# Optimization experiments

Measured on AMD Instinct MI355X. Metric: run time of the kernel, lower is better.

Reference implementation:

```python
import jax, jax.numpy as jnp
import numpy as np

N = 100000   # nodes
E = 1600000  # edges
IN = 32      # in_channels
H = 64       # hidden_channels
L = 16       # latent_dim
G = 64       # graphs in batch


def setup_inputs() -> dict:
    key = jax.random.key(0)
    ks = jax.random.split(key, 20)
    def w(k, shape, fan):
        return jax.random.normal(k, shape, jnp.float32) * (1.0 / np.sqrt(fan))
    inp = {}
    inp["x"] = jax.random.normal(ks[0], (N, IN), jnp.float32)
    inp["edge_index"] = jax.random.randint(ks[1], (2, E), 0, N)
    inp["batch"] = jnp.sort(jax.random.randint(ks[2], (N,), 0, G))
    # encoder GCN convs: in->h, h->h, h->h
    inp["W_enc0"] = w(ks[3], (IN, H), IN); inp["b_enc0"] = jnp.zeros((H,), jnp.float32)
    inp["W_enc1"] = w(ks[4], (H, H), H);   inp["b_enc1"] = jnp.zeros((H,), jnp.float32)
    inp["W_enc2"] = w(ks[5], (H, H), H);   inp["b_enc2"] = jnp.zeros((H,), jnp.float32)
    # latent projection and decoder projection
    inp["W_proj"] = w(ks[6], (H, L), H);   inp["b_proj"] = jnp.zeros((L,), jnp.float32)
    inp["W_dec_proj"] = w(ks[7], (L, H), L); inp["b_dec_proj"] = jnp.zeros((H,), jnp.float32)
    # decoder GCN convs: h->h, h->in
    inp["W_dec0"] = w(ks[8], (H, H), H);   inp["b_dec0"] = jnp.zeros((H,), jnp.float32)
    inp["W_dec1"] = w(ks[9], (H, IN), H);  inp["b_dec1"] = jnp.zeros((IN,), jnp.float32)
    return inp


def gcn_conv(x, W, b, src, dst, dinv):
    xw = x @ W                                   # [N, out]
    coef = (dinv[src] * dinv[dst])[:, None]      # [E, 1]
    out = jax.ops.segment_sum(xw[src] * coef, dst, num_segments=N)
    out = out + xw * (dinv * dinv)[:, None]      # self-loop contribution
    return out + b


def reference(x, edge_index, batch,
              W_enc0, b_enc0, W_enc1, b_enc1, W_enc2, b_enc2,
              W_proj, b_proj, W_dec_proj, b_dec_proj,
              W_dec0, b_dec0, W_dec1, b_dec1):
    src, dst = edge_index[0], edge_index[1]
    # degree with self-loops (computed on target nodes, PyG default)
    deg = jax.ops.segment_sum(jnp.ones((E,), jnp.float32), dst, num_segments=N) + 1.0
    dinv = jax.lax.rsqrt(deg)
    # encoder (eval mode: dropout is identity)
    h = jax.nn.relu(gcn_conv(x, W_enc0, b_enc0, src, dst, dinv))
    h = jax.nn.relu(gcn_conv(h, W_enc1, b_enc1, src, dst, dinv))
    h = jax.nn.relu(gcn_conv(h, W_enc2, b_enc2, src, dst, dinv))
    # global mean pool over graph ids
    sums = jax.ops.segment_sum(h, batch, num_segments=G)
    cnt = jax.ops.segment_sum(jnp.ones((N,), jnp.float32), batch, num_segments=G)
    g = sums / jnp.maximum(cnt, 1.0)[:, None]    # [G, H]
    z = g @ W_proj + b_proj                      # [G, L]
    # decoder: broadcast z back to nodes, project, two GCN convs
    d = jax.nn.relu(z[batch] @ W_dec_proj + b_dec_proj)
    d = jax.nn.relu(gcn_conv(d, W_dec0, b_dec0, src, dst, dinv))
    x_recon = gcn_conv(d, W_dec1, b_dec1, src, dst, dinv)
    return (x_recon, z)
```

## Files before the change

kernel.cpp:

```cpp
#include <hip/hip_runtime.h>
#include <hip/hip_bf16.h>

typedef unsigned long long u64;

static constexpr int IN_CH  = 32;
static constexpr int HID    = 64;
static constexpr int LAT    = 16;
static constexpr int NGRAPH = 64;
static constexpr int NBUCKET = 1024;
static constexpr int KB_CSR  = 24;


__device__ inline void add4(float4& a, const float4& b) {
    a.x += b.x; a.y += b.y; a.z += b.z; a.w += b.w;
}
__device__ inline float4 shfl_xor_f4(float4 v, int mask) {
    float4 r;
    r.x = __shfl_xor(v.x, mask);
    r.y = __shfl_xor(v.y, mask);
    r.z = __shfl_xor(v.z, mask);
    r.w = __shfl_xor(v.w, mask);
    return r;
}


__global__ __launch_bounds__(256) void bhist_kernel(const int* __restrict__ ei,
                                                    int* __restrict__ bh, int E) {
    __shared__ int lh[256];
    lh[threadIdx.x] = 0;
    __syncthreads();
    int base = blockIdx.x * 2048;
    #pragma unroll
    for (int j = 0; j < 8; j++) {
        int idx = base + j * 256 + threadIdx.x;
        if (idx < E) atomicAdd(&lh[ei[E + idx] >> 9], 1);
    }
    __syncthreads();
    if (lh[threadIdx.x]) atomicAdd(&bh[threadIdx.x], lh[threadIdx.x]);
}

__global__ __launch_bounds__(256) void bscan_kernel(const int* __restrict__ bh,
                                                    int* __restrict__ bbase, int E) {
    __shared__ int s[256];
    int t = threadIdx.x;
    int v = bh[t];
    s[t] = v;
    for (int off = 1; off < 256; off <<= 1) {
        __syncthreads();
        int x = (t >= off) ? s[t - off] : 0;
        __syncthreads();
        s[t] += x;
    }
    __syncthreads();
    bbase[t] = s[t] - v;
    if (t == 255) bbase[256] = E;
}


template <int MODE>
__global__ __launch_bounds__(256) void bin_kernel(
        const int* __restrict__ ei, const u64* __restrict__ sin,
        const int* __restrict__ rank,
        const int* __restrict__ bbase, int* __restrict__ gcur,
        u64* __restrict__ sout, int E) {
    __shared__ int lhist[256], lscan[256], lcur[256], gbase[256];
    __shared__ u64 sbuf[2048];
    int tid = threadIdx.x;
    lhist[tid] = 0;
    __syncthreads();
    int base = blockIdx.x * 2048;
    int cnt = min(2048, E - base);
    int myb[8]; u64 myp[8];
    #pragma unroll
    for (int j = 0; j < 8; j++) {
        int idx = base + j * 256 + tid;
        myb[j] = -1;
        if (idx < E) {
            int key, val;
            if constexpr (MODE == 0) { key = ei[E + idx]; val = ei[idx]; }
            else {
                u64 p = sin[idx];
                key = rank[(int)(p >> 32)];
                val = rank[(int)(p & 0xffffffffu)];
            }
            int b = key >> 9;
            myb[j] = b;
            myp[j] = ((u64)(unsigned)key << 32) | (unsigned)val;
            atomicAdd(&lhist[b], 1);
        }
    }
    __syncthreads();
    int v = lhist[tid];
    lscan[tid] = v;
    for (int off = 1; off < 256; off <<= 1) {
        __syncthreads();
        int x = (tid >= off) ? lscan[tid - off] : 0;
        __syncthreads();
        lscan[tid] += x;
    }
    __syncthreads();
    int excl = lscan[tid] - v;
    __syncthreads();
    lscan[tid] = excl;
    lcur[tid] = excl;
    __syncthreads();
    #pragma unroll
    for (int j = 0; j < 8; j++) {
        if (myb[j] >= 0) {
            int pos = atomicAdd(&lcur[myb[j]], 1);
            sbuf[pos] = myp[j];
        }
    }
    gbase[tid] = v ? atomicAdd(&gcur[tid], v) : 0;
    __syncthreads();
    for (int i = tid; i < cnt; i += 256) {
        u64 p = sbuf[i];
        int b = (int)(p >> 41);
        sout[bbase[b] + gbase[b] + (i - lscan[b])] = p;
    }
}


__global__ __launch_bounds__(256) void degb_kernel(
        const u64* __restrict__ staged, const int* __restrict__ bbase,
        int* __restrict__ cnt, int* __restrict__ hist, int N) {
    __shared__ int ldeg[512];
    __shared__ int lhist[NBUCKET];
    int b = blockIdx.x;
    ldeg[threadIdx.x] = 0;
    ldeg[threadIdx.x + 256] = 0;
    for (int i = threadIdx.x; i < NBUCKET; i += 256) lhist[i] = 0;
    __syncthreads();
    int s0 = bbase[b], s1 = bbase[b + 1];
    for (int i = s0 + threadIdx.x; i < s1; i += 256)
        atomicAdd(&ldeg[(int)(staged[i] >> 32) - (b << 9)], 1);
    __syncthreads();
    #pragma unroll
    for (int j = 0; j < 2; j++) {
        int t = threadIdx.x + j * 256;
        int n = (b << 9) + t;
        if (n < N) {
            int d = ldeg[t];
            cnt[n] = d;
            atomicAdd(&lhist[min(d, NBUCKET - 1)], 1);
        }
    }
    __syncthreads();
    for (int i = threadIdx.x; i < NBUCKET; i += 256)
        if (lhist[i]) atomicAdd(&hist[i], lhist[i]);
}

__global__ __launch_bounds__(1024) void hscan_kernel(int* hist) {
    __shared__ int s[NBUCKET];
    int t = threadIdx.x;
    int v = hist[t];
    s[t] = v;
    for (int off = 1; off < NBUCKET; off <<= 1) {
        __syncthreads();
        int x = (t >= off) ? s[t - off] : 0;
        __syncthreads();
        s[t] += x;
    }
    hist[t] = s[t] - v;
}

__global__ __launch_bounds__(256) void scatter_kernel(
        const int* __restrict__ cnt, const int* __restrict__ batch,
        const int* __restrict__ hoff, int* __restrict__ hcur,
        int* __restrict__ perm, int* __restrict__ rank, int* __restrict__ cnt2,
        float* __restrict__ dinvR, float2* __restrict__ pgR, int N) {
    __shared__ int lh[NBUCKET];
    __shared__ int gb[NBUCKET];
    for (int i = threadIdx.x; i < NBUCKET; i += 256) lh[i] = 0;
    __syncthreads();
    int n = blockIdx.x * 256 + threadIdx.x;
    int b = -1, lpos = 0, d = 0;
    if (n < N) {
        d = cnt[n];
        b = min(d, NBUCKET - 1);
        lpos = atomicAdd(&lh[b], 1);
    }
    __syncthreads();
    for (int i = threadIdx.x; i < NBUCKET; i += 256)
        gb[i] = lh[i] ? atomicAdd(&hcur[i], lh[i]) : 0;
    __syncthreads();
    if (n < N) {
        int r = hoff[b] + gb[b] + lpos;
        perm[r] = n;
        rank[n] = r;
        cnt2[r] = d;
        float dv = rsqrtf((float)d + 1.0f);
        dinvR[r] = dv;
        pgR[r] = make_float2(dv, __int_as_float(batch[n]));
    }
}


__global__ void scan1_kernel(const int* __restrict__ cnt, int* __restrict__ rowptr,
                             int* __restrict__ bsum, int N) {
    __shared__ int s[256];
    int i = blockIdx.x * 256 + threadIdx.x;
    int v = (i < N) ? cnt[i] : 0;
    s[threadIdx.x] = v;
    for (int off = 1; off < 256; off <<= 1) {
        __syncthreads();
        int t = (threadIdx.x >= off) ? s[threadIdx.x - off] : 0;
        __syncthreads();
        s[threadIdx.x] += t;
    }
    if (i < N) rowptr[i] = s[threadIdx.x] - v;
    if (threadIdx.x == 255) bsum[blockIdx.x] = s[255];
}

__global__ __launch_bounds__(512) void scan2_kernel(int* bsum, int nb) {
    __shared__ int s[512];
    int t = threadIdx.x;
    int v = (t < nb) ? bsum[t] : 0;
    s[t] = v;
    for (int off = 1; off < 512; off <<= 1) {
        __syncthreads();
        int x = (t >= off) ? s[t - off] : 0;
        __syncthreads();
        s[t] += x;
    }
    if (t < nb) bsum[t] = s[t] - v;
}

__global__ void scan3_kernel(int* __restrict__ rowptr, const int* __restrict__ bsum,
                             int* __restrict__ bbaseR, int N, int E) {
    int i = blockIdx.x * 256 + threadIdx.x;
    if (i < N) {
        int v = rowptr[i] + bsum[blockIdx.x];
        rowptr[i] = v;
        if ((i & 511) == 0) bbaseR[i >> 9] = v;
    }
    if (i == 0) {
        for (int t = (N + 511) >> 9; t <= 256; ++t) bbaseR[t] = E;
    }
}


__global__ __launch_bounds__(256) void csr_kernel(
        const u64* __restrict__ staged, const int* __restrict__ bbase,
        const int* __restrict__ rowptr2, int* __restrict__ cur,
        int* __restrict__ col) {
    int bucket = blockIdx.x & 255;
    int k = blockIdx.x >> 8;
    int s0 = bbase[bucket], s1 = bbase[bucket + 1];
    for (int i = s0 + k * 256 + threadIdx.x; i < s1; i += 256 * KB_CSR) {
        u64 p = staged[i];
        int r = (int)(p >> 32);
        int pos = rowptr2[r] + atomicAdd(&cur[r], 1);
        col[pos] = (int)(p & 0xffffffffu);
    }
}


__global__ void slice_x_kernel(const float* __restrict__ x, const int* __restrict__ perm,
                               const float* __restrict__ dinvR,
                               float* __restrict__ xs, int N) {
    int idx = blockIdx.x * 256 + threadIdx.x;
    if (idx >= N * 2) return;
    int r = idx >> 1, h = idx & 1;
    int sl = blockIdx.y;
    int n = perm[r];
    float4 v = ((const float4*)x)[(size_t)n * 8 + sl * 2 + h];
    float dn = dinvR[r];
    v.x *= dn; v.y *= dn; v.z *= dn; v.w *= dn;
    ((float4*)(xs + (size_t)sl * N * 8))[idx] = v;
}


template <int C, bool ADD_BIAS, bool OUT_ROWMAJOR>
__global__ __launch_bounds__(256) void agg_kernel(
        const float* __restrict__ in, float* __restrict__ out,
        const int* __restrict__ rowptr2, const int* __restrict__ cnt2,
        const int* __restrict__ col, const float* __restrict__ dinvR,
        const int* __restrict__ perm, const float* __restrict__ bias, int N) {
    constexpr int NSL = C / 8;
    int sl = blockIdx.x % NSL;
    int chunk = blockIdx.x / NSL;
    int slot = threadIdx.x >> 1, e = threadIdx.x & 1;
    int r = chunk * 128 + slot;
    if (r >= N) return;
    const float4* inS = (const float4*)(in + (size_t)sl * N * 8);
    int start = rowptr2[r], m = cnt2[r];
    const int* cp = col + start;
    float4 a0 = make_float4(0.f, 0.f, 0.f, 0.f);
    float4 a1 = make_float4(0.f, 0.f, 0.f, 0.f);
    {
        float4 s = inS[(size_t)r * 2 + e];
        if (e == 0) a0 = s; else a1 = s;
    }
    int i = 0;
    for (; i + 8 <= m; i += 8) {
        const int* q = cp + i + 4 * e;
        int c0 = q[0], c1 = q[1], c2 = q[2], c3 = q[3];
        float4 u0 = inS[(size_t)c0 * 2],     u1 = inS[(size_t)c1 * 2];
        float4 u2 = inS[(size_t)c2 * 2],     u3 = inS[(size_t)c3 * 2];
        float4 v0 = inS[(size_t)c0 * 2 + 1], v1 = inS[(size_t)c1 * 2 + 1];
        float4 v2 = inS[(size_t)c2 * 2 + 1], v3 = inS[(size_t)c3 * 2 + 1];
        add4(a0, u0); add4(a0, u1); add4(a0, u2); add4(a0, u3);
        add4(a1, v0); add4(a1, v1); add4(a1, v2); add4(a1, v3);
    }
    {
        int j0 = i + 4 * e;
        int j1 = min(m, j0 + 4);
        for (int j = j0; j < j1; ++j) {
            int c = cp[j];
            add4(a0, inS[(size_t)c * 2]);
            add4(a1, inS[(size_t)c * 2 + 1]);
        }
    }
    float4 sendv = e ? a0 : a1;
    float4 recv = shfl_xor_f4(sendv, 1);
    float4 tot = e ? a1 : a0;
    add4(tot, recv);
    float dn = dinvR[r];
    tot.x *= dn; tot.y *= dn; tot.z *= dn; tot.w *= dn;
    if (ADD_BIAS) {
        float4 b4 = ((const float4*)bias)[sl * 2 + e];
        add4(tot, b4);
    }
    if (OUT_ROWMAJOR) ((float4*)out)[(size_t)perm[r] * (C / 4) + sl * 2 + e] = tot;
    else ((float4*)(out + (size_t)sl * N * 8))[(size_t)r * 2 + e] = tot;
}


__global__ __launch_bounds__(256) void gagg_kernel(
        const float* __restrict__ dg, const float2* __restrict__ pgR,
        const int* __restrict__ rowptr2, const int* __restrict__ cnt2,
        const int* __restrict__ col, float* __restrict__ out, int N) {
    __shared__ float dgL[NGRAPH * 68];
    for (int i = threadIdx.x; i < NGRAPH * 64; i += 256)
        dgL[(i >> 6) * 68 + (i & 63)] = dg[i];
    __syncthreads();
    int slot = threadIdx.x >> 1, e = threadIdx.x & 1;
    int r = blockIdx.x * 128 + slot;
    if (r >= N) return;
    const float4* dgL4 = (const float4*)dgL;
    int start = rowptr2[r], m = cnt2[r];
    const int* cp = col + start;
    float2 ps = pgR[r];
    float dn = ps.x;
    int gs = __float_as_int(ps.y);
    float4 acc[8];
    {
        const float4* rp = dgL4 + gs * 17 + e * 8;
        #pragma unroll
        for (int j = 0; j < 8; ++j) {
            float4 v = rp[j];
            acc[j] = make_float4(dn * v.x, dn * v.y, dn * v.z, dn * v.w);
        }
    }
    int i = 0;
    for (; i + 2 <= m; i += 2) {
        int c0 = cp[i], c1 = cp[i + 1];
        float2 p0 = pgR[c0], p1 = pgR[c1];
        const float4* r0 = dgL4 + __float_as_int(p0.y) * 17 + e * 8;
        const float4* r1 = dgL4 + __float_as_int(p1.y) * 17 + e * 8;
        float w0 = p0.x, w1 = p1.x;
        #pragma unroll
        for (int j = 0; j < 8; ++j) {
            float4 v0 = r0[j], v1 = r1[j];
            acc[j].x += w0 * v0.x + w1 * v1.x;
            acc[j].y += w0 * v0.y + w1 * v1.y;
            acc[j].z += w0 * v0.z + w1 * v1.z;
            acc[j].w += w0 * v0.w + w1 * v1.w;
        }
    }
    if (i < m) {
        int c0 = cp[i];
        float2 p0 = pgR[c0];
        const float4* r0 = dgL4 + __float_as_int(p0.y) * 17 + e * 8;
        float w0 = p0.x;
        #pragma unroll
        for (int j = 0; j < 8; ++j) {
            float4 v0 = r0[j];
            acc[j].x += w0 * v0.x; acc[j].y += w0 * v0.y;
            acc[j].z += w0 * v0.z; acc[j].w += w0 * v0.w;
        }
    }
    #pragma unroll
    for (int k = 0; k < 4; ++k) {
        #pragma unroll
        for (int jj = 0; jj < 2; ++jj) {
            float4 v = acc[k * 2 + jj];
            v.x *= dn; v.y *= dn; v.z *= dn; v.w *= dn;
            ((float4*)(out + (size_t)(4 * e + k) * N * 8))[(size_t)r * 2 + jj] = v;
        }
    }
}


template <int CIN, int COUT, bool RELU, bool BIAS, bool SCALE, bool OUT_ROWMAJOR>
__global__ __launch_bounds__(256) void gemm_kernel(
        const float* __restrict__ in, const float* __restrict__ W,
        const float* __restrict__ b, const float* __restrict__ dinvR,
        const int* __restrict__ perm, float* __restrict__ out, int N) {
    constexpr int NPB = 256 / COUT;
    constexpr int K4 = CIN / 4;
    __shared__ float4 xsh[NPB * K4];
    int r  = threadIdx.x / COUT;
    int co = threadIdx.x % COUT;
    float w[CIN];
    #pragma unroll
    for (int k = 0; k < CIN; ++k) w[k] = W[k * COUT + co];
    float bsv = BIAS ? b[co] : 0.f;
    int ngroups = (N + NPB - 1) / NPB;
    for (int grp = blockIdx.x; grp < ngroups; grp += gridDim.x) {
        int base = grp * NPB;
        __syncthreads();
        for (int i = threadIdx.x; i < NPB * K4; i += 256) {
            int rr = i / K4, k4 = i % K4;
            int n = base + rr;
            float4 v = make_float4(0.f, 0.f, 0.f, 0.f);
            if (n < N) v = ((const float4*)(in + (size_t)(k4 >> 1) * N * 8))[(size_t)n * 2 + (k4 & 1)];
            xsh[i] = v;
        }
        __syncthreads();
        int n = base + r;
        if (n < N) {
            float acc = bsv;
            #pragma unroll
            for (int k4 = 0; k4 < K4; ++k4) {
                float4 xv = xsh[r * K4 + k4];
                acc += xv.x * w[4 * k4] + xv.y * w[4 * k4 + 1]
                     + xv.z * w[4 * k4 + 2] + xv.w * w[4 * k4 + 3];
            }
            if (RELU) acc = fmaxf(acc, 0.f);
            if (SCALE) acc *= dinvR[n];
            if (OUT_ROWMAJOR) out[(size_t)perm[n] * COUT + co] = acc;
            else out[(size_t)(co >> 3) * N * 8 + (size_t)n * 8 + (co & 7)] = acc;
        }
    }
}


__global__ __launch_bounds__(256) void pool_kernel(
        const float* __restrict__ h, const int* __restrict__ batch,
        float* __restrict__ sums, int* __restrict__ cntb, int N) {
    const int CHUNK = 512;
    int chunkStart = blockIdx.x * CHUNK;
    int c = threadIdx.x & 63;
    int r = threadIdx.x >> 6;
    int curg = -1;
    float acc = 0.f;
    int cnt = 0;
    int end = chunkStart + CHUNK;
    if (end > N) end = N;
    for (int n = chunkStart + r; n < end; n += 4) {
        int g = batch[n];
        if (g != curg) {
            if (curg >= 0) {
                atomicAdd(&sums[curg * 64 + c], acc);
                if (c == 0) atomicAdd(&cntb[curg], cnt);
            }
            curg = g; acc = 0.f; cnt = 0;
        }
        acc += h[(size_t)n * 64 + c];
        cnt++;
    }
    if (curg >= 0) {
        atomicAdd(&sums[curg * 64 + c], acc);
        if (c == 0) atomicAdd(&cntb[curg], cnt);
    }
}


__global__ __launch_bounds__(1024) void latent_kernel(
        const float* __restrict__ sums, const int* __restrict__ cntb,
        const float* __restrict__ Wp, const float* __restrict__ bp,
        const float* __restrict__ Wd, const float* __restrict__ bd,
        float* __restrict__ z_out, float* __restrict__ dg) {
    __shared__ float zl[NGRAPH * LAT];
    int t = threadIdx.x;
    {
        int g = t / LAT, l = t % LAT;
        float cf = (float)cntb[g];
        float inv = 1.0f / fmaxf(cf, 1.0f);
        float acc = bp[l];
        #pragma unroll
        for (int k = 0; k < HID; k++) acc += sums[g * HID + k] * inv * Wp[k * LAT + l];
        zl[t] = acc;
        z_out[t] = acc;
    }
    __syncthreads();
    #pragma unroll
    for (int i = 0; i < 4; i++) {
        int idx = t + i * 1024;
        int g = idx >> 6, c = idx & 63;
        float acc = bd[c];
        #pragma unroll
        for (int l = 0; l < LAT; l++) acc += zl[g * LAT + l] * Wd[l * HID + c];
        dg[idx] = fmaxf(acc, 0.f);
    }
}


extern "C" void kernel_launch(void* const* d_in, const int* in_sizes, int n_in,
                              void* d_out, int out_size, void* d_ws, size_t ws_size,
                              hipStream_t stream) {
    const float* x          = (const float*)d_in[0];
    const int*   ei         = (const int*)d_in[1];
    const int*   batch      = (const int*)d_in[2];
    const float* W_enc0     = (const float*)d_in[3];
    const float* b_enc0     = (const float*)d_in[4];
    const float* W_enc1     = (const float*)d_in[5];
    const float* b_enc1     = (const float*)d_in[6];
    const float* W_enc2     = (const float*)d_in[7];
    const float* b_enc2     = (const float*)d_in[8];
    const float* W_proj     = (const float*)d_in[9];
    const float* b_proj     = (const float*)d_in[10];
    const float* W_dec_proj = (const float*)d_in[11];
    const float* b_dec_proj = (const float*)d_in[12];
    const float* W_dec0     = (const float*)d_in[13];
    const float* b_dec0     = (const float*)d_in[14];
    const float* W_dec1     = (const float*)d_in[15];
    const float* b_dec1     = (const float*)d_in[16];

    const int N = in_sizes[0] / IN_CH;
    const int E = in_sizes[1] / 2;

    char* ws = (char*)d_ws;
    size_t off = 0;
    auto alloc = [&](size_t bytes) {
        void* p = ws + off;
        off += (bytes + 255) & ~(size_t)255;
        return p;
    };
    float* A       = (float*)alloc((size_t)N * HID * 4);
    float* B       = (float*)alloc((size_t)N * HID * 4);
    float* XS      = (float*)alloc((size_t)N * IN_CH * 4);
    int*   col     = (int*)  alloc((size_t)E * 4);
    int*   cntn    = (int*)  alloc((size_t)N * 4);
    int*   cnt2    = (int*)  alloc((size_t)N * 4);
    int*   rowptr2 = (int*)  alloc((size_t)(N + 1) * 4);
    int*   perm    = (int*)  alloc((size_t)N * 4);
    int*   rank    = (int*)  alloc((size_t)N * 4);
    float* dinvR   = (float*)alloc((size_t)N * 4);
    float2* pgR    = (float2*)alloc((size_t)N * 8);
    int nb = (N + 255) / 256;
    int*   bsum    = (int*)  alloc((size_t)nb * 4);
    int*   bbaseD  = (int*)  alloc(257 * 4);
    int*   bbaseR  = (int*)  alloc(257 * 4);
    char* zbase = ws + off;
    int*   cursor  = (int*)  alloc((size_t)N * 4);
    int*   hist    = (int*)  alloc((size_t)NBUCKET * 4);
    int*   hcur    = (int*)  alloc((size_t)NBUCKET * 4);
    int*   bh      = (int*)  alloc(256 * 4);
    int*   gcurD   = (int*)  alloc(256 * 4);
    int*   gcurR   = (int*)  alloc(256 * 4);
    float* sums    = (float*)alloc((size_t)NGRAPH * HID * 4);
    int*   cntb    = (int*)  alloc((size_t)NGRAPH * 4);
    size_t zbytes = (size_t)((ws + off) - zbase);
    float* dg      = (float*)alloc((size_t)NGRAPH * HID * 4);

    u64* staged1 = (u64*)XS;
    u64* staged2 = (u64*)A;

    float* x_recon = (float*)d_out;
    float* z_out   = (float*)d_out + (size_t)N * IN_CH;

    hipMemsetAsync(zbase, 0, zbytes, stream);

    int ebins = (E + 2047) / 2048;
    int chunks = (N + 127) / 128;

    bhist_kernel<<<ebins, 256, 0, stream>>>(ei, bh, E);
    bscan_kernel<<<1, 256, 0, stream>>>(bh, bbaseD, E);
    bin_kernel<0><<<ebins, 256, 0, stream>>>(ei, nullptr, nullptr, bbaseD, gcurD, staged1, E);
    degb_kernel<<<256, 256, 0, stream>>>(staged1, bbaseD, cntn, hist, N);
    hscan_kernel<<<1, NBUCKET, 0, stream>>>(hist);
    scatter_kernel<<<nb, 256, 0, stream>>>(cntn, batch, hist, hcur, perm, rank, cnt2,
                                           dinvR, pgR, N);
    scan1_kernel<<<nb, 256, 0, stream>>>(cnt2, rowptr2, bsum, N);
    scan2_kernel<<<1, 512, 0, stream>>>(bsum, nb);
    scan3_kernel<<<nb, 256, 0, stream>>>(rowptr2, bsum, bbaseR, N, E);
    bin_kernel<1><<<ebins, 256, 0, stream>>>(nullptr, staged1, rank, bbaseR, gcurR, staged2, E);
    csr_kernel<<<256 * KB_CSR, 256, 0, stream>>>(staged2, bbaseR, rowptr2, cursor, col);

    {
        dim3 g((N * 2 + 255) / 256, IN_CH / 8);
        slice_x_kernel<<<g, 256, 0, stream>>>(x, perm, dinvR, XS, N);
    }

    agg_kernel<IN_CH, false, false><<<chunks * 4, 256, 0, stream>>>(
        XS, A, rowptr2, cnt2, col, dinvR, perm, nullptr, N);
    gemm_kernel<IN_CH, HID, true, true, true, false><<<2048, 256, 0, stream>>>(
        A, W_enc0, b_enc0, dinvR, perm, B, N);
    agg_kernel<HID, false, false><<<chunks * 8, 256, 0, stream>>>(
        B, A, rowptr2, cnt2, col, dinvR, perm, nullptr, N);
    gemm_kernel<HID, HID, true, true, true, false><<<2048, 256, 0, stream>>>(
        A, W_enc1, b_enc1, dinvR, perm, B, N);
    agg_kernel<HID, false, false><<<chunks * 8, 256, 0, stream>>>(
        B, A, rowptr2, cnt2, col, dinvR, perm, nullptr, N);
    gemm_kernel<HID, HID, true, true, false, true><<<2048, 256, 0, stream>>>(
        A, W_enc2, b_enc2, dinvR, perm, B, N);

    pool_kernel<<<(N + 511) / 512, 256, 0, stream>>>(B, batch, sums, cntb, N);
    latent_kernel<<<1, 1024, 0, stream>>>(sums, cntb, W_proj, b_proj, W_dec_proj, b_dec_proj, z_out, dg);

    gagg_kernel<<<chunks, 256, 0, stream>>>(dg, pgR, rowptr2, cnt2, col, A, N);
    gemm_kernel<HID, HID, true, true, false, false><<<2048, 256, 0, stream>>>(
        A, W_dec0, b_dec0, dinvR, perm, B, N);
    gemm_kernel<HID, IN_CH, false, false, true, false><<<2048, 256, 0, stream>>>(
        B, W_dec1, nullptr, dinvR, perm, A, N);
    agg_kernel<IN_CH, true, true><<<chunks * 4, 256, 0, stream>>>(
        A, x_recon, rowptr2, cnt2, col, dinvR, perm, b_dec1, N);
}
```

Before: 739.9 us.

## Fold small scan kernels into consumers and rework agg column sharing

```diff
diff --git a/kernel.cpp b/kernel.cpp
--- a/kernel.cpp
+++ b/kernel.cpp
@@ -14,14 +14,6 @@
 __device__ inline void add4(float4& a, const float4& b) {
     a.x += b.x; a.y += b.y; a.z += b.z; a.w += b.w;
 }
-__device__ inline float4 shfl_xor_f4(float4 v, int mask) {
-    float4 r;
-    r.x = __shfl_xor(v.x, mask);
-    r.y = __shfl_xor(v.y, mask);
-    r.z = __shfl_xor(v.z, mask);
-    r.w = __shfl_xor(v.w, mask);
-    return r;
-}
 
 
 __global__ __launch_bounds__(256) void bhist_kernel(const int* __restrict__ ei,
@@ -39,34 +31,32 @@
     if (lh[threadIdx.x]) atomicAdd(&bh[threadIdx.x], lh[threadIdx.x]);
 }
 
-__global__ __launch_bounds__(256) void bscan_kernel(const int* __restrict__ bh,
-                                                    int* __restrict__ bbase, int E) {
-    __shared__ int s[256];
-    int t = threadIdx.x;
-    int v = bh[t];
-    s[t] = v;
-    for (int off = 1; off < 256; off <<= 1) {
-        __syncthreads();
-        int x = (t >= off) ? s[t - off] : 0;
-        __syncthreads();
-        s[t] += x;
-    }
-    __syncthreads();
-    bbase[t] = s[t] - v;
-    if (t == 255) bbase[256] = E;
-}
-
 
 template <int MODE>
 __global__ __launch_bounds__(256) void bin_kernel(
         const int* __restrict__ ei, const u64* __restrict__ sin,
         const int* __restrict__ rank,
-        const int* __restrict__ bbase, int* __restrict__ gcur,
+        const int* __restrict__ bhv,
+        int* __restrict__ gcur,
         u64* __restrict__ sout, int E) {
-    __shared__ int lhist[256], lscan[256], lcur[256], gbase[256];
+    __shared__ int lhist[256], lscan[256], lcur[256], gbase[256], bbaseL[256];
     __shared__ u64 sbuf[2048];
     int tid = threadIdx.x;
     lhist[tid] = 0;
+    if constexpr (MODE == 0) {
+        int v = bhv[tid];
+        lscan[tid] = v;
+        for (int off = 1; off < 256; off <<= 1) {
+            __syncthreads();
+            int x = (tid >= off) ? lscan[tid - off] : 0;
+            __syncthreads();
+            lscan[tid] += x;
+        }
+        __syncthreads();
+        bbaseL[tid] = lscan[tid] - v;
+    } else {
+        bbaseL[tid] = bhv[tid];
+    }
     __syncthreads();
     int base = blockIdx.x * 2048;
     int cnt = min(2048, E - base);
@@ -116,28 +106,41 @@
     for (int i = tid; i < cnt; i += 256) {
         u64 p = sbuf[i];
         int b = (int)(p >> 41);
-        sout[bbase[b] + gbase[b] + (i - lscan[b])] = p;
+        sout[bbaseL[b] + gbase[b] + (i - lscan[b])] = p;
     }
 }
 
 
 __global__ __launch_bounds__(256) void degb_kernel(
-        const u64* __restrict__ staged, const int* __restrict__ bbase,
+        const u64* __restrict__ staged, const int* __restrict__ bh,
         int* __restrict__ cnt, int* __restrict__ hist, int N) {
     __shared__ int ldeg[512];
     __shared__ int lhist[NBUCKET];
+    __shared__ int sc[256];
     int b = blockIdx.x;
-    ldeg[threadIdx.x] = 0;
-    ldeg[threadIdx.x + 256] = 0;
-    for (int i = threadIdx.x; i < NBUCKET; i += 256) lhist[i] = 0;
-    __syncthreads();
-    int s0 = bbase[b], s1 = bbase[b + 1];
-    for (int i = s0 + threadIdx.x; i < s1; i += 256)
+    int tid = threadIdx.x;
+    int bv = bh[tid];
+    sc[tid] = bv;
+    for (int off = 1; off < 256; off <<= 1) {
+        __syncthreads();
+        int x = (tid >= off) ? sc[tid - off] : 0;
+        __syncthreads();
+        sc[tid] += x;
+    }
+    __syncthreads();
+    __shared__ int s0s, s1s;
+    if (tid == b) { s0s = sc[b] - bv; s1s = sc[b]; }
+    ldeg[tid] = 0;
+    ldeg[tid + 256] = 0;
+    for (int i = tid; i < NBUCKET; i += 256) lhist[i] = 0;
+    __syncthreads();
+    int s0 = s0s, s1 = s1s;
+    for (int i = s0 + tid; i < s1; i += 256)
         atomicAdd(&ldeg[(int)(staged[i] >> 32) - (b << 9)], 1);
     __syncthreads();
     #pragma unroll
     for (int j = 0; j < 2; j++) {
-        int t = threadIdx.x + j * 256;
+        int t = tid + j * 256;
         int n = (b << 9) + t;
         if (n < N) {
             int d = ldeg[t];
@@ -146,34 +149,39 @@
         }
     }
     __syncthreads();
-    for (int i = threadIdx.x; i < NBUCKET; i += 256)
+    for (int i = tid; i < NBUCKET; i += 256)
         if (lhist[i]) atomicAdd(&hist[i], lhist[i]);
 }
 
-__global__ __launch_bounds__(1024) void hscan_kernel(int* hist) {
-    __shared__ int s[NBUCKET];
-    int t = threadIdx.x;
-    int v = hist[t];
-    s[t] = v;
-    for (int off = 1; off < NBUCKET; off <<= 1) {
-        __syncthreads();
-        int x = (t >= off) ? s[t - off] : 0;
-        __syncthreads();
-        s[t] += x;
-    }
-    hist[t] = s[t] - v;
-}
 
 __global__ __launch_bounds__(256) void scatter_kernel(
         const int* __restrict__ cnt, const int* __restrict__ batch,
-        const int* __restrict__ hoff, int* __restrict__ hcur,
+        const int* __restrict__ hist, int* __restrict__ hcur,
         int* __restrict__ perm, int* __restrict__ rank, int* __restrict__ cnt2,
         float* __restrict__ dinvR, float2* __restrict__ pgR, int N) {
     __shared__ int lh[NBUCKET];
     __shared__ int gb[NBUCKET];
-    for (int i = threadIdx.x; i < NBUCKET; i += 256) lh[i] = 0;
-    __syncthreads();
-    int n = blockIdx.x * 256 + threadIdx.x;
+    __shared__ int hoff[NBUCKET];
+    __shared__ int sc[256];
+    int tid = threadIdx.x;
+    int h0 = hist[4 * tid], h1 = hist[4 * tid + 1], h2 = hist[4 * tid + 2], h3 = hist[4 * tid + 3];
+    int T = h0 + h1 + h2 + h3;
+    sc[tid] = T;
+    for (int off = 1; off < 256; off <<= 1) {
+        __syncthreads();
+        int x = (tid >= off) ? sc[tid - off] : 0;
+        __syncthreads();
+        sc[tid] += x;
+    }
+    __syncthreads();
+    int ex = sc[tid] - T;
+    hoff[4 * tid] = ex;
+    hoff[4 * tid + 1] = ex + h0;
+    hoff[4 * tid + 2] = ex + h0 + h1;
+    hoff[4 * tid + 3] = ex + h0 + h1 + h2;
+    for (int i = tid; i < NBUCKET; i += 256) lh[i] = 0;
+    __syncthreads();
+    int n = blockIdx.x * 256 + tid;
     int b = -1, lpos = 0, d = 0;
     if (n < N) {
         d = cnt[n];
@@ -181,7 +189,7 @@
         lpos = atomicAdd(&lh[b], 1);
     }
     __syncthreads();
-    for (int i = threadIdx.x; i < NBUCKET; i += 256)
+    for (int i = tid; i < NBUCKET; i += 256)
         gb[i] = lh[i] ? atomicAdd(&hcur[i], lh[i]) : 0;
     __syncthreads();
     if (n < N) {
@@ -212,29 +220,36 @@
     if (threadIdx.x == 255) bsum[blockIdx.x] = s[255];
 }
 
-__global__ __launch_bounds__(512) void scan2_kernel(int* bsum, int nb) {
-    __shared__ int s[512];
-    int t = threadIdx.x;
-    int v = (t < nb) ? bsum[t] : 0;
-    s[t] = v;
-    for (int off = 1; off < 512; off <<= 1) {
-        __syncthreads();
-        int x = (t >= off) ? s[t - off] : 0;
-        __syncthreads();
-        s[t] += x;
-    }
-    if (t < nb) bsum[t] = s[t] - v;
-}
-
-__global__ void scan3_kernel(int* __restrict__ rowptr, const int* __restrict__ bsum,
-                             int* __restrict__ bbaseR, int N, int E) {
-    int i = blockIdx.x * 256 + threadIdx.x;
+__global__ __launch_bounds__(256) void scan3_kernel(
+        int* __restrict__ rowptr, const int* __restrict__ bsum,
+        int* __restrict__ bbaseR, int nb, int N, int E) {
+    __shared__ int sc[256];
+    int tid = threadIdx.x;
+    int v0 = (2 * tid < nb) ? bsum[2 * tid] : 0;
+    int v1 = (2 * tid + 1 < nb) ? bsum[2 * tid + 1] : 0;
+    int T = v0 + v1;
+    sc[tid] = T;
+    for (int off = 1; off < 256; off <<= 1) {
+        __syncthreads();
+        int x = (tid >= off) ? sc[tid - off] : 0;
+        __syncthreads();
+        sc[tid] += x;
+    }
+    __syncthreads();
+    __shared__ int myoff;
+    int blk = blockIdx.x;
+    if (tid == (blk >> 1)) {
+        int ex = sc[tid] - T;
+        myoff = (blk & 1) ? (ex + v0) : ex;
+    }
+    __syncthreads();
+    int i = blk * 256 + tid;
     if (i < N) {
-        int v = rowptr[i] + bsum[blockIdx.x];
+        int v = rowptr[i] + myoff;
         rowptr[i] = v;
         if ((i & 511) == 0) bbaseR[i >> 9] = v;
     }
-    if (i == 0) {
+    if (blk == 0 && tid == 0) {
         for (int t = (N + 511) >> 9; t <= 256; ++t) bbaseR[t] = E;
     }
 }
@@ -279,51 +294,45 @@
         const int* __restrict__ perm, const float* __restrict__ bias, int N) {
     constexpr int NSL = C / 8;
     int sl = blockIdx.x % NSL;
-    int chunk = blockIdx.x / NSL;
-    int slot = threadIdx.x >> 1, e = threadIdx.x & 1;
+    int nchunks = gridDim.x / NSL;
+    int chunk = nchunks - 1 - (blockIdx.x / NSL);
+    int slot = threadIdx.x >> 1, h = threadIdx.x & 1;
     int r = chunk * 128 + slot;
     if (r >= N) return;
     const float4* inS = (const float4*)(in + (size_t)sl * N * 8);
     int start = rowptr2[r], m = cnt2[r];
     const int* cp = col + start;
-    float4 a0 = make_float4(0.f, 0.f, 0.f, 0.f);
-    float4 a1 = make_float4(0.f, 0.f, 0.f, 0.f);
-    {
-        float4 s = inS[(size_t)r * 2 + e];
-        if (e == 0) a0 = s; else a1 = s;
-    }
+    float4 acc = inS[(size_t)r * 2 + h];
     int i = 0;
     for (; i + 8 <= m; i += 8) {
-        const int* q = cp + i + 4 * e;
-        int c0 = q[0], c1 = q[1], c2 = q[2], c3 = q[3];
-        float4 u0 = inS[(size_t)c0 * 2],     u1 = inS[(size_t)c1 * 2];
-        float4 u2 = inS[(size_t)c2 * 2],     u3 = inS[(size_t)c3 * 2];
-        float4 v0 = inS[(size_t)c0 * 2 + 1], v1 = inS[(size_t)c1 * 2 + 1];
-        float4 v2 = inS[(size_t)c2 * 2 + 1], v3 = inS[(size_t)c3 * 2 + 1];
-        add4(a0, u0); add4(a0, u1); add4(a0, u2); add4(a0, u3);
-        add4(a1, v0); add4(a1, v1); add4(a1, v2); add4(a1, v3);
-    }
-    {
-        int j0 = i + 4 * e;
-        int j1 = min(m, j0 + 4);
-        for (int j = j0; j < j1; ++j) {
-            int c = cp[j];
-            add4(a0, inS[(size_t)c * 2]);
-            add4(a1, inS[(size_t)c * 2 + 1]);
-        }
-    }
-    float4 sendv = e ? a0 : a1;
-    float4 recv = shfl_xor_f4(sendv, 1);
-    float4 tot = e ? a1 : a0;
-    add4(tot, recv);
+        int4 cv = *(const int4*)(cp + i + 4 * h);
+        int4 ov;
+        ov.x = __shfl_xor(cv.x, 1);
+        ov.y = __shfl_xor(cv.y, 1);
+        ov.z = __shfl_xor(cv.z, 1);
+        ov.w = __shfl_xor(cv.w, 1);
+        int4 lo = h ? ov : cv;
+        int4 hi = h ? cv : ov;
+        float4 v0 = inS[(size_t)lo.x * 2 + h], v1 = inS[(size_t)lo.y * 2 + h];
+        float4 v2 = inS[(size_t)lo.z * 2 + h], v3 = inS[(size_t)lo.w * 2 + h];
+        float4 v4 = inS[(size_t)hi.x * 2 + h], v5 = inS[(size_t)hi.y * 2 + h];
+        float4 v6 = inS[(size_t)hi.z * 2 + h], v7 = inS[(size_t)hi.w * 2 + h];
+        add4(v0, v1); add4(v2, v3); add4(v4, v5); add4(v6, v7);
+        add4(v0, v2); add4(v4, v6);
+        add4(acc, v0); add4(acc, v4);
+    }
+    for (; i < m; ++i) {
+        int c = cp[i];
+        add4(acc, inS[(size_t)c * 2 + h]);
+    }
     float dn = dinvR[r];
-    tot.x *= dn; tot.y *= dn; tot.z *= dn; tot.w *= dn;
+    acc.x *= dn; acc.y *= dn; acc.z *= dn; acc.w *= dn;
     if (ADD_BIAS) {
-        float4 b4 = ((const float4*)bias)[sl * 2 + e];
-        add4(tot, b4);
-    }
-    if (OUT_ROWMAJOR) ((float4*)out)[(size_t)perm[r] * (C / 4) + sl * 2 + e] = tot;
-    else ((float4*)(out + (size_t)sl * N * 8))[(size_t)r * 2 + e] = tot;
+        float4 b4 = ((const float4*)bias)[sl * 2 + h];
+        add4(acc, b4);
+    }
+    if (OUT_ROWMAJOR) ((float4*)out)[(size_t)perm[r] * (C / 4) + sl * 2 + h] = acc;
+    else ((float4*)(out + (size_t)sl * N * 8))[(size_t)r * 2 + h] = acc;
 }
 
 
@@ -336,7 +345,7 @@
         dgL[(i >> 6) * 68 + (i & 63)] = dg[i];
     __syncthreads();
     int slot = threadIdx.x >> 1, e = threadIdx.x & 1;
-    int r = blockIdx.x * 128 + slot;
+    int r = (gridDim.x - 1 - blockIdx.x) * 128 + slot;
     if (r >= N) return;
     const float4* dgL4 = (const float4*)dgL;
     int start = rowptr2[r], m = cnt2[r];
@@ -542,7 +551,6 @@
     float2* pgR    = (float2*)alloc((size_t)N * 8);
     int nb = (N + 255) / 256;
     int*   bsum    = (int*)  alloc((size_t)nb * 4);
-    int*   bbaseD  = (int*)  alloc(257 * 4);
     int*   bbaseR  = (int*)  alloc(257 * 4);
     char* zbase = ws + off;
     int*   cursor  = (int*)  alloc((size_t)N * 4);
@@ -568,15 +576,12 @@
     int chunks = (N + 127) / 128;
 
     bhist_kernel<<<ebins, 256, 0, stream>>>(ei, bh, E);
-    bscan_kernel<<<1, 256, 0, stream>>>(bh, bbaseD, E);
-    bin_kernel<0><<<ebins, 256, 0, stream>>>(ei, nullptr, nullptr, bbaseD, gcurD, staged1, E);
-    degb_kernel<<<256, 256, 0, stream>>>(staged1, bbaseD, cntn, hist, N);
-    hscan_kernel<<<1, NBUCKET, 0, stream>>>(hist);
+    bin_kernel<0><<<ebins, 256, 0, stream>>>(ei, nullptr, nullptr, bh, gcurD, staged1, E);
+    degb_kernel<<<256, 256, 0, stream>>>(staged1, bh, cntn, hist, N);
     scatter_kernel<<<nb, 256, 0, stream>>>(cntn, batch, hist, hcur, perm, rank, cnt2,
                                            dinvR, pgR, N);
     scan1_kernel<<<nb, 256, 0, stream>>>(cnt2, rowptr2, bsum, N);
-    scan2_kernel<<<1, 512, 0, stream>>>(bsum, nb);
-    scan3_kernel<<<nb, 256, 0, stream>>>(rowptr2, bsum, bbaseR, N, E);
+    scan3_kernel<<<nb, 256, 0, stream>>>(rowptr2, bsum, bbaseR, nb, N, E);
     bin_kernel<1><<<ebins, 256, 0, stream>>>(nullptr, staged1, rank, bbaseR, gcurR, staged2, E);
     csr_kernel<<<256 * KB_CSR, 256, 0, stream>>>(staged2, bbaseR, rowptr2, cursor, col);
 
```

Result: faster. 699.0 us (-5.5%).
